# Optimization experiments

Measured on AMD Instinct MI355X. Metric: run time of the kernel, lower is better.

The kernel has to match this reference:

```python
import jax, jax.numpy as jnp
import numpy as np

B, S, IN = 1024, 256, 8
H = 512
F = 96  # forecast_len
OUT = 1


def _lstm_step(h, c, x, Wih, Whh, bih, bhh):
    # PyTorch gate order: i, f, g, o
    gates = x @ Wih.T + h @ Whh.T + (bih + bhh)  # [B, 4H]
    i, f, g, o = jnp.split(gates, 4, axis=-1)
    i = jax.nn.sigmoid(i)
    f = jax.nn.sigmoid(f)
    g = jnp.tanh(g)
    o = jax.nn.sigmoid(o)
    c_new = f * c + i * g
    h_new = o * jnp.tanh(c_new)
    return h_new, c_new


def setup_inputs() -> dict:
    key = jax.random.key(0)
    ks = jax.random.split(key, 12)
    s_in = 1.0 / np.sqrt(H)
    def u(k, shape):
        return jax.random.uniform(k, shape, jnp.float32, -s_in, s_in)
    return {
        "x": jax.random.normal(ks[0], (B, S, IN), jnp.float32),
        "enc_Wih": u(ks[1], (4 * H, IN)),
        "enc_Whh": u(ks[2], (4 * H, H)),
        "enc_bih": u(ks[3], (4 * H,)),
        "enc_bhh": u(ks[4], (4 * H,)),
        "dec_Wih": u(ks[5], (4 * H, OUT)),
        "dec_Whh": u(ks[6], (4 * H, H)),
        "dec_bih": u(ks[7], (4 * H,)),
        "dec_bhh": u(ks[8], (4 * H,)),
        "out_W": u(ks[9], (OUT, H)),
        "out_b": u(ks[10], (OUT,)),
    }


def reference(x, enc_Wih, enc_Whh, enc_bih, enc_bhh,
              dec_Wih, dec_Whh, dec_bih, dec_bhh, out_W, out_b):
    batch = x.shape[0]
    h0 = jnp.zeros((batch, H), x.dtype)
    c0 = jnp.zeros((batch, H), x.dtype)

    # ---- Encoder: scan over time ----
    def enc_step(carry, xt):
        h, c = carry
        h, c = _lstm_step(h, c, xt, enc_Wih, enc_Whh, enc_bih, enc_bhh)
        return (h, c), None

    xs = jnp.swapaxes(x, 0, 1)  # [S, B, IN]
    (h, c), _ = jax.lax.scan(enc_step, (h0, c0), xs)

    y0 = jnp.zeros((batch, OUT), x.dtype)

    def dec_step(carry, _):
        h, c, y = carry
        h, c = _lstm_step(h, c, y, dec_Wih, dec_Whh, dec_bih, dec_bhh)
        pred = h @ out_W.T + out_b  # [B, 1]
        return (h, c, pred), pred

    _, preds = jax.lax.scan(dec_step, (h, c, y0), None, length=F)  # [F, B, 1]
    return jnp.swapaxes(preds[..., 0], 0, 1)  # [B, F]
```

## Files before the change

kernel.cpp:

```cpp
#include <hip/hip_runtime.h>


#define Hh 512
#define K2 544
#define BATCH 1024
#define SEQ 256
#define FCAST 96
#define Mrows 64
#define SAS 552
#define SHS 40

typedef _Float16 f16;
typedef _Float16 f16x8 __attribute__((ext_vector_type(8)));
typedef float f32x4 __attribute__((ext_vector_type(4)));

__device__ __forceinline__ float sigf(float v) { return 1.0f / (1.0f + __expf(-v)); }
__device__ __forceinline__ float tanhf_(float v) { return 1.0f - 2.0f / (__expf(2.0f * v) + 1.0f); }

__device__ __forceinline__ f16x8 ld16(const f16* p, bool byp) {
  f16x8 d;
  if (byp) asm volatile("global_load_dwordx4 %0, %1, off sc0 sc1" : "=v"(d) : "v"(p) : "memory");
  else     asm volatile("global_load_dwordx4 %0, %1, off sc0"     : "=v"(d) : "v"(p) : "memory");
  return d;
}
__device__ __forceinline__ void st16(f16* p, f16x8 v, bool byp) {
  if (byp) asm volatile("global_store_dwordx4 %0, %1, off sc0 sc1" :: "v"(p), "v"(v) : "memory");
  else     asm volatile("global_store_dwordx4 %0, %1, off"         :: "v"(p), "v"(v) : "memory");
}
__device__ __forceinline__ int atomic_add_l2(int* p, int v) {
  int old;
  asm volatile("global_atomic_add %0, %1, %2, off sc0\n\ts_waitcnt vmcnt(0)"
               : "=v"(old) : "v"(p), "v"(v) : "memory");
  return old;
}

__global__ void prep_weights(const float* __restrict__ encWih, const float* __restrict__ encWhh,
                             const float* __restrict__ decWih, const float* __restrict__ decWhh,
                             const float* __restrict__ encBih, const float* __restrict__ encBhh,
                             const float* __restrict__ decBih, const float* __restrict__ decBhh,
                             const float* __restrict__ outW, const float* __restrict__ outB,
                             f16* __restrict__ encT, f16* __restrict__ decPW, f16* __restrict__ decFW,
                             float* __restrict__ bE, float* __restrict__ bP, float* __restrict__ bF) {
  int id = blockIdx.x * 256 + threadIdx.x;
  if (id >= 2048 * 68) return;
  int n = id / 68, c8 = id % 68;
  int nslot = n >> 7, c = n & 127, w = c >> 5, cc = c & 31, ct = cc >> 4, l4v = cc & 15;
  int g = ct * 2 + (l4v >> 3), j = l4v & 7;
  int unit = nslot * 32 + w * 8 + j, r = g * Hh + unit;
  size_t o = (size_t)n * K2 + c8 * 8;
  if (c8 < 64) {
    float dwih = decWih[r];
#pragma unroll
    for (int e = 0; e < 8; ++e) {
      int k = c8 * 8 + e;
      encT[o + e] = (f16)encWhh[(size_t)r * Hh + k];
      float dw = decWhh[(size_t)r * Hh + k];
      decPW[o + e] = (f16)dw;
      decFW[o + e] = (f16)(dw + outW[k] * dwih);
    }
  } else if (c8 == 64) {
#pragma unroll
    for (int e = 0; e < 8; ++e) {
      encT[o + e] = (f16)encWih[r * 8 + e];
      decPW[o + e] = (f16)0.f;
      decFW[o + e] = (f16)0.f;
    }
  } else {
#pragma unroll
    for (int e = 0; e < 8; ++e) {
      encT[o + e] = (f16)0.f;
      decPW[o + e] = (f16)0.f;
      decFW[o + e] = (f16)0.f;
    }
  }
  if (c8 == 0) {
    bE[n] = encBih[r] + encBhh[r];
    float bd = decBih[r] + decBhh[r];
    bP[n] = bd;
    bF[n] = bd + outB[0] * decWih[r];
  }
}

__global__ void init_state(f16* __restrict__ h0, float* __restrict__ out,
                           const float* __restrict__ outB, int* __restrict__ sync) {
  int i = blockIdx.x * 256 + threadIdx.x;
  if (i < BATCH * Hh) h0[i] = (f16)0.f;
  if (i < BATCH * FCAST) out[i] = outB[0];
  if (i < 2048) sync[i] = 0;
}

__global__ __launch_bounds__(256, 1) void lstm_persist(
    const f16* __restrict__ encT, const f16* __restrict__ decPW, const f16* __restrict__ decFW,
    const float* __restrict__ bE, const float* __restrict__ bP, const float* __restrict__ bF,
    const float* __restrict__ x, f16* __restrict__ h0, f16* __restrict__ h1,
    float* __restrict__ out, const float* __restrict__ outW, int* __restrict__ sync) {
  __shared__ __align__(16) f16 sA[Mrows * SAS];
  __shared__ __align__(16) f16 sH[Mrows * SHS];
  __shared__ int sInfo[2];

  int* cnt = sync;
  int* slots = sync + 1024;
  int* arrive = sync + 1032;

  const int T = threadIdx.x;
  const int w = T >> 6, lane = T & 63, l4 = lane & 15, q = lane >> 4;
  const int j = l4 & 7;
  const bool lo = (l4 < 8);

  int xcd;
  asm("s_getreg_b32 %0, hwreg(HW_REG_XCC_ID)" : "=s"(xcd));
  xcd &= 7;

  if (T == 0) {
    int r = __hip_atomic_fetch_add(&slots[xcd], 1, __ATOMIC_RELAXED, __HIP_MEMORY_SCOPE_AGENT);
    sInfo[0] = r;
    __hip_atomic_fetch_add(arrive, 1, __ATOMIC_RELAXED, __HIP_MEMORY_SCOPE_AGENT);
    while (__hip_atomic_load(arrive, __ATOMIC_RELAXED, __HIP_MEMORY_SCOPE_AGENT) < 256)
      __builtin_amdgcn_s_sleep(2);
    int ok = 1;
    for (int xx = 0; xx < 8; ++xx)
      ok &= (__hip_atomic_load(&slots[xx], __ATOMIC_RELAXED, __HIP_MEMORY_SCOPE_AGENT) == 32);
    sInfo[1] = ok;
  }
  __syncthreads();
  const int rank = sInfo[0];
  const bool uni = (sInfo[1] != 0);
  int group, nslot;
  if (uni) { group = xcd * 2 + (rank >> 4); nslot = rank & 15; }
  else     { group = (int)blockIdx.x >> 4;  nslot = (int)blockIdx.x & 15; }
  const int m0 = group * Mrows, n0 = nslot * 128, u0 = nslot * 32;
  int* myCnt = cnt + group * 32;

  f16x8 bw[2][17];
  float bias_r[4];
  float cst[2][4];
#pragma unroll
  for (int a = 0; a < 2; ++a)
#pragma unroll
    for (int r = 0; r < 4; ++r) cst[a][r] = 0.f;

  const int myUnit = u0 + w * 8 + j;

  auto loadB = [&](const f16* WT, const float* bias) {
#pragma unroll
    for (int ct = 0; ct < 2; ++ct) {
      const f16* base = &WT[(size_t)(n0 + w * 32 + ct * 16 + l4) * K2 + q * 8];
#pragma unroll
      for (int ks = 0; ks < 17; ++ks) bw[ct][ks] = *(const f16x8*)(base + ks * 32);
    }
#pragma unroll
    for (int g = 0; g < 4; ++g)
      bias_r[g] = bias[n0 + w * 32 + (g >> 1) * 16 + (g & 1) * 8 + j];
  };

  loadB(encT, bE);
  float ow_r = 0.f;

  for (int s = 0; s < SEQ + FCAST; ++s) {
    const bool enc = s < SEQ;
    if (s == SEQ) {
      loadB(decPW, bP);
      ow_r = outW[myUnit];
    } else if (s == SEQ + 1) {
      loadB(decFW, bF);
    }

    if (s > 0) {
      asm volatile("s_waitcnt vmcnt(0)" ::: "memory");
      __syncthreads();
      if (T == 0) {
        if (uni) {
          atomic_add_l2(myCnt, 1);
          while (atomic_add_l2(myCnt, 0) < 16 * s) __builtin_amdgcn_s_sleep(1);
        } else {
          __hip_atomic_fetch_add(myCnt, 1, __ATOMIC_RELAXED, __HIP_MEMORY_SCOPE_AGENT);
          while (__hip_atomic_load(myCnt, __ATOMIC_RELAXED, __HIP_MEMORY_SCOPE_AGENT) < 16 * s)
            __builtin_amdgcn_s_sleep(2);
        }
      }
      __syncthreads();
    }

    const f16* hin = (s & 1) ? h1 : h0;
    f16* hout = (s & 1) ? h0 : h1;

#pragma unroll
    for (int b = 0; b < 2; ++b) {
      f16x8 d[8];
#pragma unroll
      for (int jj = 0; jj < 8; ++jj) {
        int id = T + 256 * (b * 8 + jj);
        int row = id >> 6, c8 = (id & 63) * 8;
        d[jj] = ld16(&hin[(size_t)(m0 + row) * Hh + c8], !uni);
      }
      asm volatile("s_waitcnt vmcnt(0)" ::: "memory");
#pragma unroll
      for (int jj = 0; jj < 8; ++jj) {
        int id = T + 256 * (b * 8 + jj);
        int row = id >> 6, c8 = (id & 63) * 8;
        *(f16x8*)&sA[row * SAS + c8] = d[jj];
      }
    }
    if (enc && T < Mrows) {
      const float* xp = &x[((size_t)(m0 + T) * SEQ + s) * 8];
      float4 xa = *(const float4*)xp, xb = *(const float4*)(xp + 4);
      f16x8 xv = {(f16)xa.x, (f16)xa.y, (f16)xa.z, (f16)xa.w,
                  (f16)xb.x, (f16)xb.y, (f16)xb.z, (f16)xb.w};
      f16x8 z = {(f16)0.f, (f16)0.f, (f16)0.f, (f16)0.f, (f16)0.f, (f16)0.f, (f16)0.f, (f16)0.f};
      *(f16x8*)&sA[T * SAS + 512] = xv;
      *(f16x8*)&sA[T * SAS + 520] = z;
      *(f16x8*)&sA[T * SAS + 528] = z;
      *(f16x8*)&sA[T * SAS + 536] = z;
    }
    __syncthreads();

    f32x4 acc[4][2];
#pragma unroll
    for (int a = 0; a < 4; ++a)
#pragma unroll
      for (int c = 0; c < 2; ++c) acc[a][c] = (f32x4){0.f, 0.f, 0.f, 0.f};

    auto innerK = [&](int ks) {
      int ko = ks * 32 + q * 8;
#pragma unroll
      for (int at = 0; at < 4; ++at) {
        f16x8 af = *(const f16x8*)&sA[(at * 16 + l4) * SAS + ko];
        acc[at][0] = __builtin_amdgcn_mfma_f32_16x16x32_f16(af, bw[0][ks], acc[at][0], 0, 0, 0);
        acc[at][1] = __builtin_amdgcn_mfma_f32_16x16x32_f16(af, bw[1][ks], acc[at][1], 0, 0, 0);
      }
    };
    if (enc) {
#pragma unroll
      for (int ks = 0; ks < 17; ++ks) innerK(ks);
    } else {
#pragma unroll
      for (int ks = 0; ks < 16; ++ks) innerK(ks);
    }

#pragma unroll
    for (int ah = 0; ah < 2; ++ah) {
#pragma unroll
      for (int r = 0; r < 4; ++r) {
        int atL = ah;
        int atH = ah + 2;
        float xiL = acc[atL][0][r], xgL = acc[atL][1][r];
        float xiH = acc[atH][0][r], xgH = acc[atH][1][r];
        float pf_recv = __shfl_xor(lo ? xiL : xiH, 8, 16);
        float po_recv = 0.f;
        {
          float payload0 = lo ? xiH : xiL;
          float payload1 = lo ? xgH : xgL;
          pf_recv = __shfl_xor(payload0, 8, 16);
          po_recv = __shfl_xor(payload1, 8, 16);
        }
        float gi = lo ? xiL : pf_recv;
        float gf = lo ? pf_recv : xiH;
        float gg_ = lo ? xgL : po_recv;
        float go = lo ? po_recv : xgH;
        float pi = gi + bias_r[0];
        float pf = gf + bias_r[1];
        float pg = gg_ + bias_r[2];
        float po = go + bias_r[3];
        float ig = sigf(pi), fg = sigf(pf), gg = tanhf_(pg), og = sigf(po);
        float cn = fg * cst[ah][r] + ig * gg;
        cst[ah][r] = cn;
        float hn = og * tanhf_(cn);
        int at = lo ? atL : atH;
        int row = at * 16 + q * 4 + r;
        sH[row * SHS + w * 8 + j] = (f16)hn;
        if (!enc) {
          float pp = hn * ow_r;
          pp += __shfl_xor(pp, 1, 16);
          pp += __shfl_xor(pp, 2, 16);
          pp += __shfl_xor(pp, 4, 16);
          if (j == 0) atomicAdd(&out[(m0 + row) * FCAST + (s - SEQ)], pp);
        }
      }
    }
    __syncthreads();

    {
      int row = T >> 2, seg = T & 3;
      f16x8 hv = *(const f16x8*)&sH[row * SHS + seg * 8];
      st16(&hout[(size_t)(m0 + row) * Hh + u0 + seg * 8], hv, !uni);
    }
  }
}

extern "C" void kernel_launch(void* const* d_in, const int* in_sizes, int n_in, void* d_out,
                              int out_size, void* d_ws, size_t ws_size, hipStream_t stream) {
  const float* x = (const float*)d_in[0];
  const float* encWih = (const float*)d_in[1];
  const float* encWhh = (const float*)d_in[2];
  const float* encBih = (const float*)d_in[3];
  const float* encBhh = (const float*)d_in[4];
  const float* decWih = (const float*)d_in[5];
  const float* decWhh = (const float*)d_in[6];
  const float* decBih = (const float*)d_in[7];
  const float* decBhh = (const float*)d_in[8];
  const float* outW = (const float*)d_in[9];
  const float* outB = (const float*)d_in[10];
  float* out = (float*)d_out;

  char* ws = (char*)d_ws;
  f16* encT = (f16*)ws;
  f16* decPW = encT + 2048 * K2;
  f16* decFW = decPW + 2048 * K2;
  f16* h0 = decFW + 2048 * K2;
  f16* h1 = h0 + BATCH * Hh;
  float* bE = (float*)(h1 + BATCH * Hh);
  float* bP = bE + 2048;
  float* bF = bP + 2048;
  int* sync = (int*)(bF + 2048);

  prep_weights<<<544, 256, 0, stream>>>(encWih, encWhh, decWih, decWhh, encBih, encBhh, decBih,
                                        decBhh, outW, outB, encT, decPW, decFW, bE, bP, bF);
  init_state<<<2048, 256, 0, stream>>>(h0, out, outB, sync);
  lstm_persist<<<256, 256, 0, stream>>>(encT, decPW, decFW, bE, bP, bF, x, h0, h1, out, outW, sync);
}
```

Measured before the change: 2.628 ms.

## Store hidden state in MFMA fragment layout and load directly into registers

The hidden state buffer is rearranged into an MFMA-fragment-ordered layout, so each lane can load its A-operand fragments straight from global memory into registers. This removes the per-step staging through shared memory (sA) and the barrier that followed it. The x input term is now built per lane as a separate MFMA. Loads are issued in batches with waits interleaved between MFMAs, which trades LDS traffic and a sync for more global load latency sitting on the critical path of each step.

```diff
diff --git a/kernel.cpp b/kernel.cpp
--- a/kernel.cpp
+++ b/kernel.cpp
@@ -6,9 +6,8 @@
 #define BATCH 1024
 #define SEQ 256
 #define FCAST 96
-#define Mrows 64
-#define SAS 552
 #define SHS 40
+#define HBP (16 * 64 * 64 * 8)
 
 typedef _Float16 f16;
 typedef _Float16 f16x8 __attribute__((ext_vector_type(8)));
@@ -19,8 +18,8 @@
 
 __device__ __forceinline__ f16x8 ld16(const f16* p, bool byp) {
   f16x8 d;
-  if (byp) asm volatile("global_load_dwordx4 %0, %1, off sc0 sc1" : "=v"(d) : "v"(p) : "memory");
-  else     asm volatile("global_load_dwordx4 %0, %1, off sc0"     : "=v"(d) : "v"(p) : "memory");
+  if (byp) asm volatile("global_load_dwordx4 %0, %1, off sc0 sc1" : "=&v"(d) : "v"(p) : "memory");
+  else     asm volatile("global_load_dwordx4 %0, %1, off sc0"     : "=&v"(d) : "v"(p) : "memory");
   return d;
 }
 __device__ __forceinline__ void st16(f16* p, f16x8 v, bool byp) {
@@ -32,6 +31,11 @@
   asm volatile("global_atomic_add %0, %1, %2, off sc0\n\ts_waitcnt vmcnt(0)"
                : "=v"(old) : "v"(p), "v"(v) : "memory");
   return old;
+}
+__device__ __forceinline__ void wait_frags(f16x8 (&fr)[2][4]) {
+  asm volatile("s_waitcnt vmcnt(0)"
+               : "+v"(fr[0][0]), "+v"(fr[0][1]), "+v"(fr[0][2]), "+v"(fr[0][3]),
+                 "+v"(fr[1][0]), "+v"(fr[1][1]), "+v"(fr[1][2]), "+v"(fr[1][3]));
 }
 
 __global__ void prep_weights(const float* __restrict__ encWih, const float* __restrict__ encWhh,
@@ -81,10 +85,11 @@
   }
 }
 
-__global__ void init_state(f16* __restrict__ h0, float* __restrict__ out,
+__global__ void init_state(f16* __restrict__ hbuf, float* __restrict__ out,
                            const float* __restrict__ outB, int* __restrict__ sync) {
   int i = blockIdx.x * 256 + threadIdx.x;
-  if (i < BATCH * Hh) h0[i] = (f16)0.f;
+  unsigned int* hb = (unsigned int*)hbuf;
+  if (i < 524288) hb[i] = 0u;
   if (i < BATCH * FCAST) out[i] = outB[0];
   if (i < 2048) sync[i] = 0;
 }
@@ -92,10 +97,9 @@
 __global__ __launch_bounds__(256, 1) void lstm_persist(
     const f16* __restrict__ encT, const f16* __restrict__ decPW, const f16* __restrict__ decFW,
     const float* __restrict__ bE, const float* __restrict__ bP, const float* __restrict__ bF,
-    const float* __restrict__ x, f16* __restrict__ h0, f16* __restrict__ h1,
-    float* __restrict__ out, const float* __restrict__ outW, int* __restrict__ sync) {
-  __shared__ __align__(16) f16 sA[Mrows * SAS];
-  __shared__ __align__(16) f16 sH[Mrows * SHS];
+    const float* __restrict__ x, const float* __restrict__ outW,
+    f16* __restrict__ hbuf, float* __restrict__ out, int* __restrict__ sync) {
+  __shared__ __align__(16) f16 sH[64 * SHS];
   __shared__ int sInfo[2];
 
   int* cnt = sync;
@@ -128,7 +132,7 @@
   int group, nslot;
   if (uni) { group = xcd * 2 + (rank >> 4); nslot = rank & 15; }
   else     { group = (int)blockIdx.x >> 4;  nslot = (int)blockIdx.x & 15; }
-  const int m0 = group * Mrows, n0 = nslot * 128, u0 = nslot * 32;
+  const int m0 = group * 64, n0 = nslot * 128, u0 = nslot * 32;
   int* myCnt = cnt + group * 32;
 
   f16x8 bw[2][17];
@@ -139,8 +143,6 @@
 #pragma unroll
     for (int r = 0; r < 4; ++r) cst[a][r] = 0.f;
 
-  const int myUnit = u0 + w * 8 + j;
-
   auto loadB = [&](const f16* WT, const float* bias) {
 #pragma unroll
     for (int ct = 0; ct < 2; ++ct) {
@@ -155,6 +157,8 @@
 
   loadB(encT, bE);
   float ow_r = 0.f;
+  const int myUnit = u0 + w * 8 + j;
+  const int fragBase = q * 512 + l4 * 8;
 
   for (int s = 0; s < SEQ + FCAST; ++s) {
     const bool enc = s < SEQ;
@@ -181,86 +185,69 @@
       __syncthreads();
     }
 
-    const f16* hin = (s & 1) ? h1 : h0;
-    f16* hout = (s & 1) ? h0 : h1;
-
-#pragma unroll
-    for (int b = 0; b < 2; ++b) {
-      f16x8 d[8];
-#pragma unroll
-      for (int jj = 0; jj < 8; ++jj) {
-        int id = T + 256 * (b * 8 + jj);
-        int row = id >> 6, c8 = (id & 63) * 8;
-        d[jj] = ld16(&hin[(size_t)(m0 + row) * Hh + c8], !uni);
+    const int pin = s & 1, pout = pin ^ 1;
+    const f16* hbL = hbuf + (size_t)pin * HBP + (size_t)group * 32768 + fragBase;
+    f16* hbO = hbuf + (size_t)pout * HBP + (size_t)group * 32768;
+
+    f32x4 acc[4][2];
+#pragma unroll
+    for (int a = 0; a < 4; ++a)
+#pragma unroll
+      for (int c = 0; c < 2; ++c) acc[a][c] = (f32x4){0.f, 0.f, 0.f, 0.f};
+
+#pragma unroll
+    for (int b = 0; b < 8; ++b) {
+      f16x8 fr[2][4];
+#pragma unroll
+      for (int k2 = 0; k2 < 2; ++k2)
+#pragma unroll
+        for (int at = 0; at < 4; ++at)
+          fr[k2][at] = ld16(&hbL[(b * 2 + k2) * 2048 + at * 128], !uni);
+      wait_frags(fr);
+#pragma unroll
+      for (int k2 = 0; k2 < 2; ++k2) {
+        const int ks = b * 2 + k2;
+#pragma unroll
+        for (int at = 0; at < 4; ++at) {
+          acc[at][0] =
+              __builtin_amdgcn_mfma_f32_16x16x32_f16(fr[k2][at], bw[0][ks], acc[at][0], 0, 0, 0);
+          acc[at][1] =
+              __builtin_amdgcn_mfma_f32_16x16x32_f16(fr[k2][at], bw[1][ks], acc[at][1], 0, 0, 0);
+        }
       }
-      asm volatile("s_waitcnt vmcnt(0)" ::: "memory");
-#pragma unroll
-      for (int jj = 0; jj < 8; ++jj) {
-        int id = T + 256 * (b * 8 + jj);
-        int row = id >> 6, c8 = (id & 63) * 8;
-        *(f16x8*)&sA[row * SAS + c8] = d[jj];
+    }
+
+    if (enc) {
+#pragma unroll
+      for (int at = 0; at < 4; ++at) {
+        f16x8 af = {(f16)0.f, (f16)0.f, (f16)0.f, (f16)0.f,
+                    (f16)0.f, (f16)0.f, (f16)0.f, (f16)0.f};
+        if (q == 0) {
+          const float* xp = &x[((size_t)(m0 + at * 16 + l4) * SEQ + s) * 8];
+          float4 xa = *(const float4*)xp, xb = *(const float4*)(xp + 4);
+          af = f16x8{(f16)xa.x, (f16)xa.y, (f16)xa.z, (f16)xa.w,
+                     (f16)xb.x, (f16)xb.y, (f16)xb.z, (f16)xb.w};
+        }
+        acc[at][0] = __builtin_amdgcn_mfma_f32_16x16x32_f16(af, bw[0][16], acc[at][0], 0, 0, 0);
+        acc[at][1] = __builtin_amdgcn_mfma_f32_16x16x32_f16(af, bw[1][16], acc[at][1], 0, 0, 0);
       }
     }
-    if (enc && T < Mrows) {
-      const float* xp = &x[((size_t)(m0 + T) * SEQ + s) * 8];
-      float4 xa = *(const float4*)xp, xb = *(const float4*)(xp + 4);
-      f16x8 xv = {(f16)xa.x, (f16)xa.y, (f16)xa.z, (f16)xa.w,
-                  (f16)xb.x, (f16)xb.y, (f16)xb.z, (f16)xb.w};
-      f16x8 z = {(f16)0.f, (f16)0.f, (f16)0.f, (f16)0.f, (f16)0.f, (f16)0.f, (f16)0.f, (f16)0.f};
-      *(f16x8*)&sA[T * SAS + 512] = xv;
-      *(f16x8*)&sA[T * SAS + 520] = z;
-      *(f16x8*)&sA[T * SAS + 528] = z;
-      *(f16x8*)&sA[T * SAS + 536] = z;
-    }
-    __syncthreads();
-
-    f32x4 acc[4][2];
-#pragma unroll
-    for (int a = 0; a < 4; ++a)
-#pragma unroll
-      for (int c = 0; c < 2; ++c) acc[a][c] = (f32x4){0.f, 0.f, 0.f, 0.f};
-
-    auto innerK = [&](int ks) {
-      int ko = ks * 32 + q * 8;
-#pragma unroll
-      for (int at = 0; at < 4; ++at) {
-        f16x8 af = *(const f16x8*)&sA[(at * 16 + l4) * SAS + ko];
-        acc[at][0] = __builtin_amdgcn_mfma_f32_16x16x32_f16(af, bw[0][ks], acc[at][0], 0, 0, 0);
-        acc[at][1] = __builtin_amdgcn_mfma_f32_16x16x32_f16(af, bw[1][ks], acc[at][1], 0, 0, 0);
-      }
-    };
-    if (enc) {
-#pragma unroll
-      for (int ks = 0; ks < 17; ++ks) innerK(ks);
-    } else {
-#pragma unroll
-      for (int ks = 0; ks < 16; ++ks) innerK(ks);
-    }
 
 #pragma unroll
     for (int ah = 0; ah < 2; ++ah) {
 #pragma unroll
       for (int r = 0; r < 4; ++r) {
-        int atL = ah;
-        int atH = ah + 2;
+        int atL = ah, atH = ah + 2;
         float xiL = acc[atL][0][r], xgL = acc[atL][1][r];
         float xiH = acc[atH][0][r], xgH = acc[atH][1][r];
-        float pf_recv = __shfl_xor(lo ? xiL : xiH, 8, 16);
-        float po_recv = 0.f;
-        {
-          float payload0 = lo ? xiH : xiL;
-          float payload1 = lo ? xgH : xgL;
-          pf_recv = __shfl_xor(payload0, 8, 16);
-          po_recv = __shfl_xor(payload1, 8, 16);
-        }
-        float gi = lo ? xiL : pf_recv;
-        float gf = lo ? pf_recv : xiH;
-        float gg_ = lo ? xgL : po_recv;
-        float go = lo ? po_recv : xgH;
-        float pi = gi + bias_r[0];
-        float pf = gf + bias_r[1];
-        float pg = gg_ + bias_r[2];
-        float po = go + bias_r[3];
+        float payload0 = lo ? xiH : xiL;
+        float payload1 = lo ? xgH : xgL;
+        float recv0 = __shfl_xor(payload0, 8, 16);
+        float recv1 = __shfl_xor(payload1, 8, 16);
+        float pi = (lo ? xiL : recv0) + bias_r[0];
+        float pf = (lo ? recv0 : xiH) + bias_r[1];
+        float pg = (lo ? xgL : recv1) + bias_r[2];
+        float po = (lo ? recv1 : xgH) + bias_r[3];
         float ig = sigf(pi), fg = sigf(pf), gg = tanhf_(pg), og = sigf(po);
         float cn = fg * cst[ah][r] + ig * gg;
         cst[ah][r] = cn;
@@ -280,9 +267,9 @@
     __syncthreads();
 
     {
-      int row = T >> 2, seg = T & 3;
+      int row = lane, seg = w;
       f16x8 hv = *(const f16x8*)&sH[row * SHS + seg * 8];
-      st16(&hout[(size_t)(m0 + row) * Hh + u0 + seg * 8], hv, !uni);
+      st16(&hbO[((nslot * 4 + seg) * 64 + row) * 8], hv, !uni);
     }
   }
 }
@@ -306,15 +293,14 @@
   f16* encT = (f16*)ws;
   f16* decPW = encT + 2048 * K2;
   f16* decFW = decPW + 2048 * K2;
-  f16* h0 = decFW + 2048 * K2;
-  f16* h1 = h0 + BATCH * Hh;
-  float* bE = (float*)(h1 + BATCH * Hh);
+  f16* hbuf = decFW + 2048 * K2;
+  float* bE = (float*)(hbuf + 2 * HBP);
   float* bP = bE + 2048;
   float* bF = bP + 2048;
   int* sync = (int*)(bF + 2048);
 
   prep_weights<<<544, 256, 0, stream>>>(encWih, encWhh, decWih, decWhh, encBih, encBhh, decBih,
                                         decBhh, outW, outB, encT, decPW, decFW, bE, bP, bF);
-  init_state<<<2048, 256, 0, stream>>>(h0, out, outB, sync);
-  lstm_persist<<<256, 256, 0, stream>>>(encT, decPW, decFW, bE, bP, bF, x, h0, h1, out, outW, sync);
-}
+  init_state<<<2048, 256, 0, stream>>>(hbuf, out, outB, sync);
+  lstm_persist<<<256, 256, 0, stream>>>(encT, decPW, decFW, bE, bP, bF, x, outW, hbuf, out, sync);
+}
```

New measurement: 2.718 ms. 1.03x slower.
